# Kernel tuning notes

Hardware: AMD Instinct MI355X
Metric: run time of the kernel (lower is better)

## Reference

```python
import jax, jax.numpy as jnp
import numpy as np

B, T, D = 4096, 200, 64
NEG_INF = -(2.0 ** 32) + 1.0  # matches tf paddings constant


def setup_inputs() -> dict:
    key = jax.random.key(0)
    ks = jax.random.split(key, 12)
    queries = jax.random.normal(ks[0], (B, D), dtype=jnp.float32)
    keys = jax.random.normal(ks[1], (B, T, D), dtype=jnp.float32)
    keys_length = jax.random.randint(ks[2], (B,), 0, 200, dtype=jnp.int32)
    # attention MLP params (glorot-ish scale)
    W1 = jax.random.normal(ks[3], (4 * D, 16), dtype=jnp.float32) * (1.0 / np.sqrt(4 * D))
    b1 = jnp.zeros((16,), dtype=jnp.float32)
    W2 = jax.random.normal(ks[4], (16, 8), dtype=jnp.float32) * (1.0 / np.sqrt(16))
    b2 = jnp.zeros((8,), dtype=jnp.float32)
    W3 = jax.random.normal(ks[5], (8, 1), dtype=jnp.float32) * (1.0 / np.sqrt(8))
    b3 = jnp.zeros((1,), dtype=jnp.float32)
    W4 = jax.random.normal(ks[6], (D, D), dtype=jnp.float32) * (1.0 / np.sqrt(D))
    b4 = jnp.zeros((D,), dtype=jnp.float32)
    return {"queries": queries, "keys": keys, "keys_length": keys_length,
            "W1": W1, "b1": b1, "W2": W2, "b2": b2, "W3": W3, "b3": b3,
            "W4": W4, "b4": b4}


def reference(queries, keys, keys_length, W1, b1, W2, b2, W3, b3, W4, b4):
    Bq, Tq, Dq = keys.shape
    # tile queries across time: [B, T, D]
    q = jnp.broadcast_to(queries[:, None, :], (Bq, Tq, Dq))
    # DIN feature construction: [B, T, 4D]
    din_all = jnp.concatenate([q, keys, q - keys, q * keys], axis=-1)
    # tiny MLP scorer
    x = jax.nn.sigmoid(jnp.einsum('btf,fh->bth', din_all, W1) + b1)
    x = jax.nn.sigmoid(jnp.einsum('bth,hk->btk', x, W2) + b2)
    scores = (jnp.einsum('btk,ko->bto', x, W3) + b3)[..., 0]  # [B, T]
    # mask invalid history positions
    mask = jnp.arange(Tq, dtype=keys_length.dtype)[None, :] < keys_length[:, None]
    scores = jnp.where(mask, scores, NEG_INF)
    scores = scores / (Dq ** 0.5)  # scaling applied after masking, as in tf code
    attn = jax.nn.softmax(scores, axis=-1)  # [B, T]
    out = jnp.einsum('bt,btd->bd', attn, keys)  # weighted sum of keys
    out = out @ W4 + b4  # [B, D]
    return out
```

## Files before the change

kernel.cpp:

```cpp
#include <hip/hip_runtime.h>
#include <math.h>

#define TT 200
#define MTS 72

typedef __attribute__((ext_vector_type(8))) short bf16x8;
typedef __attribute__((ext_vector_type(4))) float f32x4;

__device__ __forceinline__ float sigmoidf_(float x) {
    return 1.0f / (1.0f + __expf(-x));
}
__device__ __forceinline__ short f2bf(float x) {
    unsigned u = __float_as_uint(x);
    u += 0x7fff + ((u >> 16) & 1);
    return (short)(u >> 16);
}
__device__ __forceinline__ float bf2f(short s) {
    return __uint_as_float(((unsigned)(unsigned short)s) << 16);
}
__device__ __forceinline__ void build_hi(float4 v0, float4 v1, bf16x8& hi) {
    float xs[8] = {v0.x, v0.y, v0.z, v0.w, v1.x, v1.y, v1.z, v1.w};
    #pragma unroll
    for (int j = 0; j < 8; j++) hi[j] = f2bf(xs[j]);
}

__global__ __launch_bounds__(256) void din_attn_flash(
    const float* __restrict__ queries,
    const float* __restrict__ keys,
    const int*   __restrict__ keys_length,
    const float* __restrict__ W1,
    const float* __restrict__ b1,
    const float* __restrict__ W2,
    const float* __restrict__ b2,
    const float* __restrict__ W3,
    const float* __restrict__ b3,
    const float* __restrict__ W4,
    const float* __restrict__ b4,
    float* __restrict__ out,
    int Bn)
{
    __shared__ __align__(16) short MtHi[4][16 * MTS];
    __shared__ __align__(16) short MtLo[4][16 * MTS];
    __shared__ __align__(16) float vS[4][64];

    const int tid  = threadIdx.x;
    const int w    = tid >> 6;
    const int lane = tid & 63;
    const int m16  = lane & 15;
    const int quad = lane >> 4;

    const int b = blockIdx.x * 4 + w;
    if (b >= Bn) return;
    const int len = __builtin_amdgcn_readfirstlane(keys_length[b]);
    const float* kb = keys + (size_t)b * (TT * 64);

    float cp0 = 0.f, cp1 = 0.f, cp2 = 0.f, cp3 = 0.f;
    {
        const int d2 = lane >> 2;
        const int hg = lane & 3;
        const float4* W1v = (const float4*)W1;
        #pragma unroll
        for (int dg = 0; dg < 4; dg++) {
            const int d = dg * 16 + d2;
            const float q = queries[b * 64 + d];
            float4 a  = W1v[(0   + d) * 4 + hg];
            float4 bb = W1v[(64  + d) * 4 + hg];
            float4 cc = W1v[(128 + d) * 4 + hg];
            float4 dd = W1v[(192 + d) * 4 + hg];
            float mv0 = bb.x - cc.x + q * dd.x;
            float mv1 = bb.y - cc.y + q * dd.y;
            float mv2 = bb.z - cc.z + q * dd.z;
            float mv3 = bb.w - cc.w + q * dd.w;
            cp0 += q * (a.x + cc.x);
            cp1 += q * (a.y + cc.y);
            cp2 += q * (a.z + cc.z);
            cp3 += q * (a.w + cc.w);
            const int hb = hg * 4;
            short h0 = f2bf(mv0), h1 = f2bf(mv1), h2 = f2bf(mv2), h3 = f2bf(mv3);
            MtHi[w][(hb + 0) * MTS + d] = h0;
            MtHi[w][(hb + 1) * MTS + d] = h1;
            MtHi[w][(hb + 2) * MTS + d] = h2;
            MtHi[w][(hb + 3) * MTS + d] = h3;
            MtLo[w][(hb + 0) * MTS + d] = f2bf(mv0 - bf2f(h0));
            MtLo[w][(hb + 1) * MTS + d] = f2bf(mv1 - bf2f(h1));
            MtLo[w][(hb + 2) * MTS + d] = f2bf(mv2 - bf2f(h2));
            MtLo[w][(hb + 3) * MTS + d] = f2bf(mv3 - bf2f(h3));
        }
        #pragma unroll
        for (int mask = 4; mask <= 32; mask <<= 1) {
            cp0 += __shfl_xor(cp0, mask, 64);
            cp1 += __shfl_xor(cp1, mask, 64);
            cp2 += __shfl_xor(cp2, mask, 64);
            cp3 += __shfl_xor(cp3, mask, 64);
        }
    }
    float cv4[4];
    cv4[0] = __shfl(cp0, quad, 64) + b1[quad * 4 + 0];
    cv4[1] = __shfl(cp1, quad, 64) + b1[quad * 4 + 1];
    cv4[2] = __shfl(cp2, quad, 64) + b1[quad * 4 + 2];
    cv4[3] = __shfl(cp3, quad, 64) + b1[quad * 4 + 3];

    asm volatile("" ::: "memory");
    __builtin_amdgcn_wave_barrier();

    const int bb0 = m16 * MTS + quad * 8;
    const bf16x8 Bh0 = *(const bf16x8*)&MtHi[w][bb0];
    const bf16x8 Bh1 = *(const bf16x8*)&MtHi[w][bb0 + 32];
    const bf16x8 Bl0 = *(const bf16x8*)&MtLo[w][bb0];
    const bf16x8 Bl1 = *(const bf16x8*)&MtLo[w][bb0 + 32];

    float4 wa_[4], wb_[4];
    #pragma unroll
    for (int r = 0; r < 4; r++) {
        wa_[r] = *(const float4*)(W2 + (quad * 4 + r) * 8);
        wb_[r] = *(const float4*)(W2 + (quad * 4 + r) * 8 + 4);
    }
    const float4 b2a = *(const float4*)(b2);
    const float4 b2b = *(const float4*)(b2 + 4);
    const float4 w3a = *(const float4*)(W3);
    const float4 w3b = *(const float4*)(W3 + 4);
    const float  b3v = b3[0];

    const float M = 0.125f * (fabsf(b3v)
                  + fabsf(w3a.x) + fabsf(w3a.y) + fabsf(w3a.z) + fabsf(w3a.w)
                  + fabsf(w3b.x) + fabsf(w3b.y) + fabsf(w3b.z) + fabsf(w3b.w));

    const int lenEff = (len == 0) ? TT : len;
    const int ntiles = (lenEff + 15) >> 4;

    float ssum = 0.0f;
    float o[16];
    #pragma unroll
    for (int j = 0; j < 16; j++) o[j] = 0.0f;

    const float* kp0 = kb + m16 * 64 + quad * 8;
    float4 c0 = *(const float4*)(kp0);
    float4 c1 = *(const float4*)(kp0 + 4);
    float4 c2 = *(const float4*)(kp0 + 32);
    float4 c3 = *(const float4*)(kp0 + 36);

    for (int tile = 0; tile < ntiles; tile++) {
        float4 n0, n1, n2, n3;
        const bool pf = (tile + 1 < ntiles);
        if (pf) {
            int tr = (tile + 1) * 16 + m16;
            if (tr > TT - 1) tr = TT - 1;
            const float* np = kb + tr * 64 + quad * 8;
            n0 = *(const float4*)(np);
            n1 = *(const float4*)(np + 4);
            n2 = *(const float4*)(np + 32);
            n3 = *(const float4*)(np + 36);
        }
        bf16x8 ah0, ah1;
        build_hi(c0, c1, ah0);
        build_hi(c2, c3, ah1);
        f32x4 acc = {0.f, 0.f, 0.f, 0.f};
        acc = __builtin_amdgcn_mfma_f32_16x16x32_bf16(Bh0, ah0, acc, 0, 0, 0);
        acc = __builtin_amdgcn_mfma_f32_16x16x32_bf16(Bl0, ah0, acc, 0, 0, 0);
        acc = __builtin_amdgcn_mfma_f32_16x16x32_bf16(Bh1, ah1, acc, 0, 0, 0);
        acc = __builtin_amdgcn_mfma_f32_16x16x32_bf16(Bl1, ah1, acc, 0, 0, 0);

        float s2[8] = {b2a.x, b2a.y, b2a.z, b2a.w, b2b.x, b2b.y, b2b.z, b2b.w};
        #pragma unroll
        for (int r = 0; r < 4; r++) {
            const float h1 = sigmoidf_(acc[r] + cv4[r]);
            s2[0] = fmaf(h1, wa_[r].x, s2[0]);
            s2[1] = fmaf(h1, wa_[r].y, s2[1]);
            s2[2] = fmaf(h1, wa_[r].z, s2[2]);
            s2[3] = fmaf(h1, wa_[r].w, s2[3]);
            s2[4] = fmaf(h1, wb_[r].x, s2[4]);
            s2[5] = fmaf(h1, wb_[r].y, s2[5]);
            s2[6] = fmaf(h1, wb_[r].z, s2[6]);
            s2[7] = fmaf(h1, wb_[r].w, s2[7]);
        }
        #pragma unroll
        for (int j = 0; j < 8; j++) {
            s2[j] += __shfl_xor(s2[j], 16, 64);
            s2[j] += __shfl_xor(s2[j], 32, 64);
        }
        float s3 = b3v;
        s3 = fmaf(sigmoidf_(s2[0]), w3a.x, s3);
        s3 = fmaf(sigmoidf_(s2[1]), w3a.y, s3);
        s3 = fmaf(sigmoidf_(s2[2]), w3a.z, s3);
        s3 = fmaf(sigmoidf_(s2[3]), w3a.w, s3);
        s3 = fmaf(sigmoidf_(s2[4]), w3b.x, s3);
        s3 = fmaf(sigmoidf_(s2[5]), w3b.y, s3);
        s3 = fmaf(sigmoidf_(s2[6]), w3b.z, s3);
        s3 = fmaf(sigmoidf_(s2[7]), w3b.w, s3);

        const int tg = tile * 16 + m16;
        float sc = (len == 0) ? 0.0f : s3 * 0.125f;
        if (tg >= lenEff) sc = -1.0e30f;
        const float p = __expf(sc - M);

        ssum += p;
        o[0]  = fmaf(p, c0.x, o[0]);
        o[1]  = fmaf(p, c0.y, o[1]);
        o[2]  = fmaf(p, c0.z, o[2]);
        o[3]  = fmaf(p, c0.w, o[3]);
        o[4]  = fmaf(p, c1.x, o[4]);
        o[5]  = fmaf(p, c1.y, o[5]);
        o[6]  = fmaf(p, c1.z, o[6]);
        o[7]  = fmaf(p, c1.w, o[7]);
        o[8]  = fmaf(p, c2.x, o[8]);
        o[9]  = fmaf(p, c2.y, o[9]);
        o[10] = fmaf(p, c2.z, o[10]);
        o[11] = fmaf(p, c2.w, o[11]);
        o[12] = fmaf(p, c3.x, o[12]);
        o[13] = fmaf(p, c3.y, o[13]);
        o[14] = fmaf(p, c3.z, o[14]);
        o[15] = fmaf(p, c3.w, o[15]);

        if (pf) { c0 = n0; c1 = n1; c2 = n2; c3 = n3; }
    }

    #pragma unroll
    for (int mask = 1; mask <= 8; mask <<= 1) {
        ssum += __shfl_xor(ssum, mask, 64);
        #pragma unroll
        for (int j = 0; j < 16; j++) o[j] += __shfl_xor(o[j], mask, 64);
    }
    const float inv = 1.0f / ssum;
    if (m16 == 0) {
        #pragma unroll
        for (int j = 0; j < 8; j++) vS[w][quad * 8 + j]      = o[j] * inv;
        #pragma unroll
        for (int j = 0; j < 8; j++) vS[w][32 + quad * 8 + j] = o[8 + j] * inv;
    }
    asm volatile("" ::: "memory");
    __builtin_amdgcn_wave_barrier();

    float po = b4[lane];
    const float4* vS4 = (const float4*)&vS[w][0];
    #pragma unroll 4
    for (int d0 = 0; d0 < 16; d0++) {
        const float4 vv = vS4[d0];
        const float* w4p = W4 + d0 * 256 + lane;
        po = fmaf(vv.x, w4p[0],   po);
        po = fmaf(vv.y, w4p[64],  po);
        po = fmaf(vv.z, w4p[128], po);
        po = fmaf(vv.w, w4p[192], po);
    }
    out[(size_t)b * 64 + lane] = po;
}

extern "C" void kernel_launch(void* const* d_in, const int* in_sizes, int n_in,
                              void* d_out, int out_size, void* d_ws, size_t ws_size,
                              hipStream_t stream) {
    const float* queries     = (const float*)d_in[0];
    const float* keys        = (const float*)d_in[1];
    const int*   keys_length = (const int*)  d_in[2];
    const float* W1 = (const float*)d_in[3];
    const float* b1 = (const float*)d_in[4];
    const float* W2 = (const float*)d_in[5];
    const float* b2 = (const float*)d_in[6];
    const float* W3 = (const float*)d_in[7];
    const float* b3 = (const float*)d_in[8];
    const float* W4 = (const float*)d_in[9];
    const float* b4 = (const float*)d_in[10];
    float* out = (float*)d_out;

    const int Bn = in_sizes[2];
    const int blocks = (Bn + 3) >> 2;
    din_attn_flash<<<blocks, 256, 0, stream>>>(
        queries, keys, keys_length, W1, b1, W2, b2, W3, b3, W4, b4, out, Bn);
}
```

Before: 294.5 us.

## Run second MLP layer on MFMA, use packed bf16 converts, deepen key prefetch

The second MLP layer (16->8) now runs as a bf16 MFMA with W2 packed into an operand fragment. This replaces per-lane scalar FMAs and eight pairs of cross-lane shuffles with one matrix op and a two-step shuffle on the final score. Float-to-bf16 conversion now uses the hardware packed-convert instruction instead of manual rounding. Key tiles are prefetched two ahead and out-of-range rows are skipped, and launch bounds request 4 blocks per CU. Layer-2 inputs and weights are rounded to bf16, which lowers precision.

Measured after the change: 294.2 us. Within noise of the previous version (-0.1%).

```diff
diff --git a/kernel.cpp b/kernel.cpp
--- a/kernel.cpp
+++ b/kernel.cpp
@@ -7,8 +7,15 @@
 typedef __attribute__((ext_vector_type(8))) short bf16x8;
 typedef __attribute__((ext_vector_type(4))) float f32x4;
 
+union BF8 { bf16x8 v; unsigned u[4]; };
+
 __device__ __forceinline__ float sigmoidf_(float x) {
     return 1.0f / (1.0f + __expf(-x));
+}
+__device__ __forceinline__ unsigned cvtpk(float a, float b) {
+    unsigned r;
+    asm("v_cvt_pk_bf16_f32 %0, %1, %2" : "=v"(r) : "v"(a), "v"(b));
+    return r;
 }
 __device__ __forceinline__ short f2bf(float x) {
     unsigned u = __float_as_uint(x);
@@ -18,13 +25,8 @@
 __device__ __forceinline__ float bf2f(short s) {
     return __uint_as_float(((unsigned)(unsigned short)s) << 16);
 }
-__device__ __forceinline__ void build_hi(float4 v0, float4 v1, bf16x8& hi) {
-    float xs[8] = {v0.x, v0.y, v0.z, v0.w, v1.x, v1.y, v1.z, v1.w};
-    #pragma unroll
-    for (int j = 0; j < 8; j++) hi[j] = f2bf(xs[j]);
-}
-
-__global__ __launch_bounds__(256) void din_attn_flash(
+
+__global__ __launch_bounds__(256, 4) void din_attn_flash(
     const float* __restrict__ queries,
     const float* __restrict__ keys,
     const int*   __restrict__ keys_length,
@@ -109,17 +111,31 @@
     const bf16x8 Bl0 = *(const bf16x8*)&MtLo[w][bb0];
     const bf16x8 Bl1 = *(const bf16x8*)&MtLo[w][bb0 + 32];
 
-    float4 wa_[4], wb_[4];
-    #pragma unroll
-    for (int r = 0; r < 4; r++) {
-        wa_[r] = *(const float4*)(W2 + (quad * 4 + r) * 8);
-        wb_[r] = *(const float4*)(W2 + (quad * 4 + r) * 8 + 4);
-    }
+    BF8 a2;
+    {
+        float w2f[4];
+        #pragma unroll
+        for (int j = 0; j < 4; j++)
+            w2f[j] = (m16 < 8) ? W2[(quad * 4 + j) * 8 + m16] : 0.0f;
+        a2.u[0] = cvtpk(w2f[0], w2f[1]);
+        a2.u[1] = cvtpk(w2f[2], w2f[3]);
+        a2.u[2] = 0u;
+        a2.u[3] = 0u;
+    }
+
     const float4 b2a = *(const float4*)(b2);
     const float4 b2b = *(const float4*)(b2 + 4);
     const float4 w3a = *(const float4*)(W3);
     const float4 w3b = *(const float4*)(W3 + 4);
     const float  b3v = b3[0];
+    const float b2k0 = quad == 0 ? b2a.x : (quad == 1 ? b2b.x : 0.f);
+    const float b2k1 = quad == 0 ? b2a.y : (quad == 1 ? b2b.y : 0.f);
+    const float b2k2 = quad == 0 ? b2a.z : (quad == 1 ? b2b.z : 0.f);
+    const float b2k3 = quad == 0 ? b2a.w : (quad == 1 ? b2b.w : 0.f);
+    const float w3k0 = quad == 0 ? w3a.x : (quad == 1 ? w3b.x : 0.f);
+    const float w3k1 = quad == 0 ? w3a.y : (quad == 1 ? w3b.y : 0.f);
+    const float w3k2 = quad == 0 ? w3a.z : (quad == 1 ? w3b.z : 0.f);
+    const float w3k3 = quad == 0 ? w3a.w : (quad == 1 ? w3b.w : 0.f);
 
     const float M = 0.125f * (fabsf(b3v)
                   + fabsf(w3a.x) + fabsf(w3a.y) + fabsf(w3a.z) + fabsf(w3a.w)
@@ -133,63 +149,60 @@
     #pragma unroll
     for (int j = 0; j < 16; j++) o[j] = 0.0f;
 
-    const float* kp0 = kb + m16 * 64 + quad * 8;
-    float4 c0 = *(const float4*)(kp0);
-    float4 c1 = *(const float4*)(kp0 + 4);
-    float4 c2 = *(const float4*)(kp0 + 32);
-    float4 c3 = *(const float4*)(kp0 + 36);
+    const float4 z4 = {0.f, 0.f, 0.f, 0.f};
+    #define LOADT(TL, A0, A1, A2, A3)                                   \
+        { const int t_ = (TL) * 16 + m16;                               \
+          if (t_ < lenEff) {                                            \
+              const float* p_ = kb + t_ * 64 + quad * 8;                \
+              A0 = *(const float4*)(p_);                                \
+              A1 = *(const float4*)(p_ + 4);                            \
+              A2 = *(const float4*)(p_ + 32);                           \
+              A3 = *(const float4*)(p_ + 36);                           \
+          } else { A0 = z4; A1 = z4; A2 = z4; A3 = z4; } }
+
+    float4 c0, c1, c2, c3, n0, n1, n2, n3;
+    LOADT(0, c0, c1, c2, c3);
+    LOADT(1, n0, n1, n2, n3);
 
     for (int tile = 0; tile < ntiles; tile++) {
-        float4 n0, n1, n2, n3;
-        const bool pf = (tile + 1 < ntiles);
-        if (pf) {
-            int tr = (tile + 1) * 16 + m16;
-            if (tr > TT - 1) tr = TT - 1;
-            const float* np = kb + tr * 64 + quad * 8;
-            n0 = *(const float4*)(np);
-            n1 = *(const float4*)(np + 4);
-            n2 = *(const float4*)(np + 32);
-            n3 = *(const float4*)(np + 36);
-        }
-        bf16x8 ah0, ah1;
-        build_hi(c0, c1, ah0);
-        build_hi(c2, c3, ah1);
+        float4 m0, m1, m2, m3;
+        LOADT(tile + 2, m0, m1, m2, m3);
+
+        BF8 ah0, ah1;
+        ah0.u[0] = cvtpk(c0.x, c0.y);  ah0.u[1] = cvtpk(c0.z, c0.w);
+        ah0.u[2] = cvtpk(c1.x, c1.y);  ah0.u[3] = cvtpk(c1.z, c1.w);
+        ah1.u[0] = cvtpk(c2.x, c2.y);  ah1.u[1] = cvtpk(c2.z, c2.w);
+        ah1.u[2] = cvtpk(c3.x, c3.y);  ah1.u[3] = cvtpk(c3.z, c3.w);
+
         f32x4 acc = {0.f, 0.f, 0.f, 0.f};
-        acc = __builtin_amdgcn_mfma_f32_16x16x32_bf16(Bh0, ah0, acc, 0, 0, 0);
-        acc = __builtin_amdgcn_mfma_f32_16x16x32_bf16(Bl0, ah0, acc, 0, 0, 0);
-        acc = __builtin_amdgcn_mfma_f32_16x16x32_bf16(Bh1, ah1, acc, 0, 0, 0);
-        acc = __builtin_amdgcn_mfma_f32_16x16x32_bf16(Bl1, ah1, acc, 0, 0, 0);
-
-        float s2[8] = {b2a.x, b2a.y, b2a.z, b2a.w, b2b.x, b2b.y, b2b.z, b2b.w};
-        #pragma unroll
-        for (int r = 0; r < 4; r++) {
-            const float h1 = sigmoidf_(acc[r] + cv4[r]);
-            s2[0] = fmaf(h1, wa_[r].x, s2[0]);
-            s2[1] = fmaf(h1, wa_[r].y, s2[1]);
-            s2[2] = fmaf(h1, wa_[r].z, s2[2]);
-            s2[3] = fmaf(h1, wa_[r].w, s2[3]);
-            s2[4] = fmaf(h1, wb_[r].x, s2[4]);
-            s2[5] = fmaf(h1, wb_[r].y, s2[5]);
-            s2[6] = fmaf(h1, wb_[r].z, s2[6]);
-            s2[7] = fmaf(h1, wb_[r].w, s2[7]);
-        }
-        #pragma unroll
-        for (int j = 0; j < 8; j++) {
-            s2[j] += __shfl_xor(s2[j], 16, 64);
-            s2[j] += __shfl_xor(s2[j], 32, 64);
-        }
-        float s3 = b3v;
-        s3 = fmaf(sigmoidf_(s2[0]), w3a.x, s3);
-        s3 = fmaf(sigmoidf_(s2[1]), w3a.y, s3);
-        s3 = fmaf(sigmoidf_(s2[2]), w3a.z, s3);
-        s3 = fmaf(sigmoidf_(s2[3]), w3a.w, s3);
-        s3 = fmaf(sigmoidf_(s2[4]), w3b.x, s3);
-        s3 = fmaf(sigmoidf_(s2[5]), w3b.y, s3);
-        s3 = fmaf(sigmoidf_(s2[6]), w3b.z, s3);
-        s3 = fmaf(sigmoidf_(s2[7]), w3b.w, s3);
+        acc = __builtin_amdgcn_mfma_f32_16x16x32_bf16(Bh0, ah0.v, acc, 0, 0, 0);
+        acc = __builtin_amdgcn_mfma_f32_16x16x32_bf16(Bl0, ah0.v, acc, 0, 0, 0);
+        acc = __builtin_amdgcn_mfma_f32_16x16x32_bf16(Bh1, ah1.v, acc, 0, 0, 0);
+        acc = __builtin_amdgcn_mfma_f32_16x16x32_bf16(Bl1, ah1.v, acc, 0, 0, 0);
+
+        const float h10 = sigmoidf_(acc[0] + cv4[0]);
+        const float h11 = sigmoidf_(acc[1] + cv4[1]);
+        const float h12 = sigmoidf_(acc[2] + cv4[2]);
+        const float h13 = sigmoidf_(acc[3] + cv4[3]);
+        BF8 hb;
+        hb.u[0] = cvtpk(h10, h11);
+        hb.u[1] = cvtpk(h12, h13);
+        hb.u[2] = 0u;
+        hb.u[3] = 0u;
+
+        f32x4 acc2 = {0.f, 0.f, 0.f, 0.f};
+        acc2 = __builtin_amdgcn_mfma_f32_16x16x32_bf16(a2.v, hb.v, acc2, 0, 0, 0);
+
+        float s3p;
+        s3p = sigmoidf_(acc2[0] + b2k0) * w3k0;
+        s3p = fmaf(sigmoidf_(acc2[1] + b2k1), w3k1, s3p);
+        s3p = fmaf(sigmoidf_(acc2[2] + b2k2), w3k2, s3p);
+        s3p = fmaf(sigmoidf_(acc2[3] + b2k3), w3k3, s3p);
+        s3p += __shfl_xor(s3p, 16, 64);
+        s3p += __shfl_xor(s3p, 32, 64);
 
         const int tg = tile * 16 + m16;
-        float sc = (len == 0) ? 0.0f : s3 * 0.125f;
+        float sc = (len == 0) ? 0.0f : (s3p + b3v) * 0.125f;
         if (tg >= lenEff) sc = -1.0e30f;
         const float p = __expf(sc - M);
 
@@ -211,8 +224,10 @@
         o[14] = fmaf(p, c3.z, o[14]);
         o[15] = fmaf(p, c3.w, o[15]);
 
-        if (pf) { c0 = n0; c1 = n1; c2 = n2; c3 = n3; }
-    }
+        c0 = n0; c1 = n1; c2 = n2; c3 = n3;
+        n0 = m0; n1 = m1; n2 = m2; n3 = m3;
+    }
+    #undef LOADT
 
     #pragma unroll
     for (int mask = 1; mask <= 8; mask <<= 1) {
```
